# Kernel tuning notes

Measured on AMD Instinct MI355X. Metric: run time of the kernel, lower is better.

The kernel has to match this reference:

```python
import jax, jax.numpy as jnp
import numpy as np

BN_EPS = 0.001
ALPHA = 10.0
WEIGHT_BIT = 8
ACT_BIT = 8
BIAS_BIT = 16


def _ste_round(x, s):
    # straight-through quantize: round(x*s)/s with identity gradient
    return x + jax.lax.stop_gradient(jnp.round(x * s) / s - x)


def _qsym(x, bit):
    # symmetric per-tensor 'scale' quantization
    s = (2.0 ** (bit - 1) - 1.0) / jnp.maximum(jnp.max(jnp.abs(x)), 1e-8)
    return _ste_round(x, s)


def _qrelu(x, alpha, bit):
    # clipped ReLU to [0, alpha] then uniform quantization to 2^bit - 1 levels
    y = jnp.clip(x, 0.0, alpha)
    s = (2.0 ** bit - 1.0) / alpha
    return _ste_round(y, s)


def _folded_qconv(x, w, b, gamma, beta, mean, var, stride, pad):
    # fold BN into conv weights/bias, then quantize weight (8b) and bias (16b)
    sc = gamma / jnp.sqrt(var + BN_EPS)            # [O]
    wf = _qsym(w * sc[:, None, None, None], WEIGHT_BIT)
    bf = _qsym((b - mean) * sc + beta, BIAS_BIT)
    y = jax.lax.conv_general_dilated(
        x, wf, window_strides=stride, padding=[(pad, pad), (pad, pad)],
        dimension_numbers=('NCHW', 'OIHW', 'NCHW'))
    return y + bf[None, :, None, None]


def setup_inputs() -> dict:
    key = jax.random.key(0)
    ks = jax.random.split(key, 20)
    Cin, Cmid, Cout = 256, 128, 512
    d = {'x': jax.random.normal(ks[0], (32, Cin, 56, 56), dtype=jnp.float32)}

    def mk(k0, o, i, kh, kw, tag):
        kk = jax.random.split(k0, 6)
        fan = i * kh * kw
        d['w' + tag] = jax.random.normal(kk[0], (o, i, kh, kw), jnp.float32) * (fan ** -0.5)
        d['b' + tag] = jax.random.normal(kk[1], (o,), jnp.float32) * 0.01
        d['g' + tag] = 1.0 + jax.random.normal(kk[2], (o,), jnp.float32) * 0.1
        d['be' + tag] = jax.random.normal(kk[3], (o,), jnp.float32) * 0.1
        d['m' + tag] = jax.random.normal(kk[4], (o,), jnp.float32) * 0.1
        d['v' + tag] = jax.random.uniform(kk[5], (o,), jnp.float32) + 0.5

    mk(ks[1], Cmid, Cin, 1, 1, '1')
    mk(ks[2], Cmid, Cmid, 3, 3, '2')
    mk(ks[3], Cout, Cmid, 1, 1, '3')
    return d


def reference(x, w1, b1, g1, be1, m1, v1,
              w2, b2, g2, be2, m2, v2,
              w3, b3, g3, be3, m3, v3):
    out = _folded_qconv(x, w1, b1, g1, be1, m1, v1, (1, 1), 0)
    out = _qrelu(out, ALPHA, ACT_BIT)
    out = _folded_qconv(out, w2, b2, g2, be2, m2, v2, (1, 1), 1)
    out = _qrelu(out, ALPHA, ACT_BIT)
    out = _folded_qconv(out, w3, b3, g3, be3, m3, v3, (1, 1), 0)
    return out
```

## Files before the change

### kernel.cpp

```cpp
#include <hip/hip_runtime.h>
#include <math.h>

typedef int v4i  __attribute__((ext_vector_type(4)));
typedef int v16i __attribute__((ext_vector_type(16)));
typedef short v8s __attribute__((ext_vector_type(8)));
typedef float v16f __attribute__((ext_vector_type(16)));

#define N_IMG 32
#define CIN   256
#define CMID  128
#define COUT  512
#define HWP   3136
#define W58   58
#define PLANE_Q 3456
#define CBSTRIDE (PLANE_Q*16)
#define IMGSTRIDE (8*CBSTRIDE)
#define BSROW 248
#define GUARD 16384
#define BN_EPS_F 1e-3f
#define ALPHA_F  10.0f
#define ARELU_S  25.5f

#define OFF_WQ1   0
#define OFF_WF2   32768
#define OFF_WF3   180224
#define OFF_BQ1   245760
#define OFF_BQ2   245888
#define OFF_BQ3   246016
#define OFF_MAX   246528
#define OFF_Q2    246536
#define OFF_Q3    246664
#define OFF_WQ2I  247296
#define OFF_WQ3I  284160
#define OFF_WBF1  300544
#define ACT1Q_GUARD_B 52582400u
#define ACT1Q_B       (ACT1Q_GUARD_B + GUARD)
#define ACT2Q_B       (ACT1Q_B + (unsigned)(N_IMG*IMGSTRIDE) + GUARD)

__device__ __forceinline__ void async16(const char* g, char* l) {
    __builtin_amdgcn_global_load_lds((const __attribute__((address_space(1))) void*)g,
                                     (__attribute__((address_space(3))) void*)l, 16, 0, 0);
}

__global__ __launch_bounds__(256) void fold_all_kernel(
    const float* __restrict__ w1, const float* __restrict__ g1, const float* __restrict__ v1,
    const float* __restrict__ w2, const float* __restrict__ g2, const float* __restrict__ v2,
    const float* __restrict__ w3, const float* __restrict__ g3, const float* __restrict__ v3,
    const float* __restrict__ b1, const float* __restrict__ be1, const float* __restrict__ m1,
    const float* __restrict__ b2, const float* __restrict__ be2, const float* __restrict__ m2,
    const float* __restrict__ b3, const float* __restrict__ be3, const float* __restrict__ m3,
    float* __restrict__ wq1, float* __restrict__ wf2, float* __restrict__ wf3,
    float* __restrict__ bq1, float* __restrict__ bq2, float* __restrict__ bq3,
    unsigned int* __restrict__ maxw)
{
    __shared__ float red[256];
    const int b = blockIdx.x, t = threadIdx.x;
    if (b < 960) {
        const float *w, *g, *v; float* wf; int inner; unsigned int* mslot; int i;
        if (b < 128)      { w = w1; g = g1; v = v1; wf = wq1; inner = CIN;      mslot = maxw + 0; i = b * 256 + t; }
        else if (b < 704) { w = w2; g = g2; v = v2; wf = wf2; inner = CMID * 9; mslot = maxw + 1; i = (b - 128) * 256 + t; }
        else              { w = w3; g = g3; v = v3; wf = wf3; inner = CMID;     mslot = maxw + 2; i = (b - 704) * 256 + t; }
        int o = i / inner;
        float sc = g[o] / sqrtf(v[o] + BN_EPS_F);
        float val = w[i] * sc;
        wf[i] = val;
        red[t] = fabsf(val);
        __syncthreads();
        for (int s = 128; s > 0; s >>= 1) {
            if (t < s) red[t] = fmaxf(red[t], red[t + s]);
            __syncthreads();
        }
        if (t == 0) atomicMax(mslot, __float_as_uint(red[0]));
    } else {
        const float *bb, *gg, *bebe, *mm, *vv; float* bq; int nn;
        if (b == 960)      { bb = b1; gg = g1; bebe = be1; mm = m1; vv = v1; bq = bq1; nn = CMID; }
        else if (b == 961) { bb = b2; gg = g2; bebe = be2; mm = m2; vv = v2; bq = bq2; nn = CMID; }
        else               { bb = b3; gg = g3; bebe = be3; mm = m3; vv = v3; bq = bq3; nn = COUT; }
        float val0 = 0.f, val1 = 0.f;
        if (t < nn) {
            float sc = gg[t] / sqrtf(vv[t] + BN_EPS_F);
            val0 = (bb[t] - mm[t]) * sc + bebe[t];
        }
        int t2 = t + 256;
        if (t2 < nn) {
            float sc = gg[t2] / sqrtf(vv[t2] + BN_EPS_F);
            val1 = (bb[t2] - mm[t2]) * sc + bebe[t2];
        }
        red[t] = fmaxf(fabsf(val0), fabsf(val1));
        __syncthreads();
        for (int s = 128; s > 0; s >>= 1) {
            if (t < s) red[t] = fmaxf(red[t], red[t + s]);
            __syncthreads();
        }
        float mx = fmaxf(red[0], 1e-8f);
        float s = 32767.0f / mx;
        if (t < nn)  bq[t]  = rintf(val0 * s) / s;
        if (t2 < nn) bq[t2] = rintf(val1 * s) / s;
    }
}

__global__ __launch_bounds__(256) void quant_all_kernel(
    const float* __restrict__ wq1f, const float* __restrict__ wf2, const float* __restrict__ wf3,
    const unsigned int* __restrict__ maxw,
    unsigned short* __restrict__ wbf, char* __restrict__ wq2i, char* __restrict__ wq3i,
    int* __restrict__ Q2, int* __restrict__ Q3)
{
    __shared__ int red[256];
    const int b = blockIdx.x, t = threadIdx.x;
    if (b < 128) {
        int i = b * 256 + t;
        float s = 127.0f / fmaxf(__uint_as_float(maxw[0]), 1e-8f);
        int kb = i >> 10, rem = i & 1023;
        int m = rem >> 3, j = rem & 7;
        int c = kb * 8 + j;
        float k = rintf(wq1f[m * CIN + c] * s);
        wbf[i] = (unsigned short)(__float_as_uint(k) >> 16);
    } else if (b < 256) {
        int m = b - 128;
        float s = 127.0f / fmaxf(__uint_as_float(maxw[1]), 1e-8f);
        int sum = 0;
        for (int idx = t; idx < CMID * 9; idx += 256) {
            int c = idx / 9, tap = idx - c * 9;
            int q = (int)rintf(wf2[(size_t)m * (CMID * 9) + idx] * s);
            wq2i[(size_t)tap * 16384 + (c >> 4) * 2048 + m * 16 + (c & 15)] = (char)q;
            sum += q;
        }
        red[t] = sum;
        __syncthreads();
        for (int st = 128; st > 0; st >>= 1) {
            if (t < st) red[t] += red[t + st];
            __syncthreads();
        }
        if (t == 0) Q2[m] = red[0];
    } else {
        int m = (b - 256) * 2 + (t >> 7), c = t & 127;
        float s = 127.0f / fmaxf(__uint_as_float(maxw[2]), 1e-8f);
        int q = (int)rintf(wf3[(size_t)m * CMID + c] * s);
        wq3i[(size_t)(c >> 4) * 8192 + m * 16 + (c & 15)] = (char)q;
        red[t] = q;
        __syncthreads();
        for (int st = 64; st > 0; st >>= 1) {
            if ((t & 127) < st) red[t] += red[t + st];
            __syncthreads();
        }
        if ((t & 127) == 0) Q3[m] = red[t];
    }
}

__global__ __launch_bounds__(256) void conv1_bf16_kernel(
    const float* __restrict__ X, const unsigned short* __restrict__ Wbf,
    const unsigned int* __restrict__ maxw, const float* __restrict__ bq1,
    char* __restrict__ act1q)
{
    __shared__ char lds[49152];
    char* Bh = lds;
    char* Bm = lds + 16384;
    char* Bl = lds + 32768;
    const int tid = threadIdx.x;
    const int n  = blockIdx.z;
    const int q0 = blockIdx.x * 128;
    const int lane = tid & 63, wid = tid >> 6;
    const int lo = lane & 31, hi = lane >> 5;
    const int wm = wid >> 1, wn = wid & 1;
    const float* Xn = X + (size_t)n * CIN * HWP;

    const int skb = tid >> 5, sqq = tid & 31;
    const int qq0 = q0 + sqq * 4;
    int p_[4];
#pragma unroll
    for (int e = 0; e < 4; e++) {
        int q = qq0 + e;
        int y = q / W58, xx = q - y * W58;
        int p = (y - 1) * 56 + (xx - 1);
        p_[e] = p < 0 ? 0 : (p > HWP - 1 ? HWP - 1 : p);
    }
    const bool fast = (p_[1] == p_[0] + 1) && (p_[2] == p_[0] + 2) && (p_[3] == p_[0] + 3);

    v16f acc[2][2] = {};

    for (int kc = 0; kc < 4; kc++) {
        __syncthreads();
        const float* chbase = Xn + (size_t)(kc * 64 + skb * 8) * HWP;
        float v[8][4];
#pragma unroll
        for (int j = 0; j < 8; j++) {
            const float* cp = chbase + (size_t)j * HWP;
            if (fast) {
                float4 f = *(const float4*)(cp + p_[0]);
                v[j][0] = f.x; v[j][1] = f.y; v[j][2] = f.z; v[j][3] = f.w;
            } else {
#pragma unroll
                for (int e = 0; e < 4; e++) v[j][e] = cp[p_[e]];
            }
        }
#pragma unroll
        for (int e = 0; e < 4; e++) {
            unsigned ph[4], pm_[4], pl[4];
#pragma unroll
            for (int jj = 0; jj < 4; jj++) {
                float a0 = v[2 * jj][e], a1 = v[2 * jj + 1][e];
                unsigned u0 = __float_as_uint(a0), u1 = __float_as_uint(a1);
                unsigned h0 = u0 & 0xFFFF0000u, h1 = u1 & 0xFFFF0000u;
                float r0 = a0 - __uint_as_float(h0), r1 = a1 - __uint_as_float(h1);
                unsigned w0 = __float_as_uint(r0) & 0xFFFF0000u;
                unsigned w1 = __float_as_uint(r1) & 0xFFFF0000u;
                float s0 = r0 - __uint_as_float(w0), s1 = r1 - __uint_as_float(w1);
                unsigned l0 = __float_as_uint(s0) & 0xFFFF0000u;
                unsigned l1 = __float_as_uint(s1) & 0xFFFF0000u;
                ph[jj]  = (h0 >> 16) | h1;
                pm_[jj] = (w0 >> 16) | w1;
                pl[jj]  = (l0 >> 16) | l1;
            }
            int off = (skb * 128 + sqq * 4 + e) * 16;
            *(uint4*)(Bh + off) = make_uint4(ph[0], ph[1], ph[2], ph[3]);
            *(uint4*)(Bm + off) = make_uint4(pm_[0], pm_[1], pm_[2], pm_[3]);
            *(uint4*)(Bl + off) = make_uint4(pl[0], pl[1], pl[2], pl[3]);
        }
        __syncthreads();

        const char* wbase = (const char*)Wbf + kc * 16384;
#pragma unroll
        for (int ks = 0; ks < 4; ks++) {
            v8s a[2];
#pragma unroll
            for (int s = 0; s < 2; s++)
                a[s] = *(const v8s*)(wbase + (((ks * 2 + hi) * 128) + wm * 64 + s * 32 + lo) * 16);
#pragma unroll
            for (int pass = 0; pass < 3; pass++) {
                const char* Bp = (pass == 0) ? Bh : ((pass == 1) ? Bm : Bl);
                v8s b[2];
#pragma unroll
                for (int t = 0; t < 2; t++)
                    b[t] = *(const v8s*)(Bp + ((ks * 2 + hi) * 128 + wn * 64 + t * 32 + lo) * 16);
#pragma unroll
                for (int s = 0; s < 2; s++)
#pragma unroll
                    for (int t = 0; t < 2; t++)
                        acc[s][t] = __builtin_amdgcn_mfma_f32_32x32x16_bf16(a[s], b[t], acc[s][t], 0, 0, 0);
            }
        }
    }

    float inv_s = fmaxf(__uint_as_float(maxw[0]), 1e-8f) / 127.0f;
    __syncthreads();
    char* Cs = lds;
#pragma unroll
    for (int s = 0; s < 2; s++)
#pragma unroll
        for (int t = 0; t < 2; t++) {
            int qloc = wn * 64 + t * 32 + lo;
#pragma unroll
            for (int reg = 0; reg < 16; reg++) {
                int m = wm * 64 + s * 32 + (reg & 3) + 8 * (reg >> 2) + 4 * hi;
                float val = fmaf(acc[s][t][reg], inv_s, bq1[m]);
                val = fminf(fmaxf(val, 0.f), ALPHA_F);
                int k1 = (int)rintf(val * ARELU_S);
                Cs[qloc * 148 + m] = (char)(k1 - 128);
            }
        }
    __syncthreads();
    char* dst = act1q + (size_t)n * IMGSTRIDE + (size_t)q0 * 16;
#pragma unroll
    for (int it = 0; it < 4; it++) {
        int idx = it * 256 + tid;
        int ql = idx >> 3, cb = idx & 7;
        int q = q0 + ql;
        int y = q / W58, xx = q - y * W58;
        int4 w;
        if ((unsigned)(y - 1) < 56u && (unsigned)(xx - 1) < 56u) {
            w.x = *(const int*)(Cs + ql * 148 + cb * 16 + 0);
            w.y = *(const int*)(Cs + ql * 148 + cb * 16 + 4);
            w.z = *(const int*)(Cs + ql * 148 + cb * 16 + 8);
            w.w = *(const int*)(Cs + ql * 148 + cb * 16 + 12);
        } else {
            w = make_int4(0x80808080, 0x80808080, 0x80808080, 0x80808080);
        }
        *(int4*)(dst + (size_t)cb * CBSTRIDE + ql * 16) = w;
    }
}

__global__ __launch_bounds__(256) void conv2_i8_kernel(
    const char* __restrict__ actq, const char* __restrict__ wq2i,
    const int* __restrict__ Q2, const float* __restrict__ bq2,
    const unsigned int* __restrict__ maxw, char* __restrict__ act2q)
{
    __shared__ char lds[31744];
    char* Bs = lds;
    const int tid = threadIdx.x;
    const int n  = blockIdx.z;
    const int q0 = blockIdx.x * 128;
    const int lane = tid & 63, wid = tid >> 6;
    const int lo = lane & 31, hi = lane >> 5;
    const int wm = wid >> 1, wn = wid & 1;

    const char* src = actq + (size_t)n * IMGSTRIDE + (long)(q0 - 59) * 16;
#pragma unroll
    for (int cb = 0; cb < 8; cb++) {
        if (tid < 246)
            async16(src + (size_t)cb * CBSTRIDE + tid * 16, Bs + cb * (BSROW * 16) + tid * 16);
    }
    __syncthreads();

    v16i acc[2][2] = {};
    for (int tap = 0; tap < 9; tap++) {
        const char* wt = wq2i + (size_t)tap * 16384;
        const int tapoff = ((tap / 3) - 1) * W58 + (tap % 3) - 1;
#pragma unroll
        for (int ks = 0; ks < 4; ks++) {
            v4i a[2], b[2];
#pragma unroll
            for (int s = 0; s < 2; s++)
                a[s] = *(const v4i*)(wt + (ks * 2 + hi) * 2048 + (wm * 64 + s * 32 + lo) * 16);
#pragma unroll
            for (int t = 0; t < 2; t++) {
                int ql = 59 + tapoff + wn * 64 + t * 32 + lo;
                b[t] = *(const v4i*)(Bs + ((ks * 2 + hi) * BSROW + ql) * 16);
            }
#pragma unroll
            for (int s = 0; s < 2; s++)
#pragma unroll
                for (int t = 0; t < 2; t++)
                    acc[s][t] = __builtin_amdgcn_mfma_i32_32x32x32_i8(a[s], b[t], acc[s][t], 0, 0, 0);
        }
    }

    float scale = fmaxf(__uint_as_float(maxw[1]), 1e-8f) / (127.0f * ARELU_S);
    __syncthreads();
    char* Cs = lds;
#pragma unroll
    for (int s = 0; s < 2; s++)
#pragma unroll
        for (int t = 0; t < 2; t++) {
            int qloc = wn * 64 + t * 32 + lo;
#pragma unroll
            for (int reg = 0; reg < 16; reg++) {
                int m = wm * 64 + s * 32 + (reg & 3) + 8 * (reg >> 2) + 4 * hi;
                float val = fmaf((float)(acc[s][t][reg] + 128 * Q2[m]), scale, bq2[m]);
                val = fminf(fmaxf(val, 0.f), ALPHA_F);
                int k2 = (int)rintf(val * ARELU_S);
                Cs[qloc * 148 + m] = (char)(k2 - 128);
            }
        }
    __syncthreads();
    char* dst = act2q + (size_t)n * IMGSTRIDE + q0 * 16;
#pragma unroll
    for (int it = 0; it < 4; it++) {
        int idx = it * 256 + tid;
        int q = idx >> 3, cb = idx & 7;
        int4 w;
        w.x = *(const int*)(Cs + q * 148 + cb * 16 + 0);
        w.y = *(const int*)(Cs + q * 148 + cb * 16 + 4);
        w.z = *(const int*)(Cs + q * 148 + cb * 16 + 8);
        w.w = *(const int*)(Cs + q * 148 + cb * 16 + 12);
        *(int4*)(dst + (size_t)cb * CBSTRIDE + q * 16) = w;
    }
}

__global__ __launch_bounds__(256) void conv3_i8_kernel(
    const char* __restrict__ act2q, const char* __restrict__ wq3i,
    const int* __restrict__ Q3, const float* __restrict__ bq3,
    const unsigned int* __restrict__ maxw, float* __restrict__ out)
{
    __shared__ char lds[16384];
    char* Bs = lds;
    const int tid = threadIdx.x;
    const int n  = blockIdx.z;
    const int q0 = blockIdx.x * 128;
    const int m0 = blockIdx.y * 128;
    const int lane = tid & 63, wid = tid >> 6;
    const int lo = lane & 31, hi = lane >> 5;
    const int wm = wid >> 1, wn = wid & 1;

    const char* bsrc = act2q + (size_t)n * IMGSTRIDE + q0 * 16;
#pragma unroll
    for (int i = 0; i < 4; i++) {
        int cb = i * 2 + (tid >> 7), row = tid & 127;
        async16(bsrc + (size_t)cb * CBSTRIDE + row * 16, Bs + cb * 2048 + row * 16);
    }
    __syncthreads();

    v16i acc[2][2] = {};
#pragma unroll
    for (int ks = 0; ks < 4; ks++) {
        v4i a[2], b[2];
#pragma unroll
        for (int s = 0; s < 2; s++)
            a[s] = *(const v4i*)(wq3i + (ks * 2 + hi) * 8192 + (m0 + wm * 64 + s * 32 + lo) * 16);
#pragma unroll
        for (int t = 0; t < 2; t++)
            b[t] = *(const v4i*)(Bs + ((ks * 2 + hi) * 128 + wn * 64 + t * 32 + lo) * 16);
#pragma unroll
        for (int s = 0; s < 2; s++)
#pragma unroll
            for (int t = 0; t < 2; t++)
                acc[s][t] = __builtin_amdgcn_mfma_i32_32x32x32_i8(a[s], b[t], acc[s][t], 0, 0, 0);
    }

    float scale = fmaxf(__uint_as_float(maxw[2]), 1e-8f) / (127.0f * ARELU_S);
#pragma unroll
    for (int s = 0; s < 2; s++)
#pragma unroll
        for (int t = 0; t < 2; t++) {
            int q = q0 + wn * 64 + t * 32 + lo;
            int y = q / W58, x = q - y * W58;
            if ((unsigned)(y - 1) < 56u && (unsigned)(x - 1) < 56u) {
                int p = (y - 1) * 56 + (x - 1);
                float* op = out + (size_t)n * COUT * HWP + p;
#pragma unroll
                for (int reg = 0; reg < 16; reg++) {
                    int m = m0 + wm * 64 + s * 32 + (reg & 3) + 8 * (reg >> 2) + 4 * hi;
                    op[(size_t)m * HWP] = fmaf((float)(acc[s][t][reg] + 128 * Q3[m]), scale, bq3[m]);
                }
            }
        }
}

extern "C" void kernel_launch(void* const* d_in, const int* in_sizes, int n_in,
                              void* d_out, int out_size, void* d_ws, size_t ws_size,
                              hipStream_t stream) {
    const float* x   = (const float*)d_in[0];
    const float* w1  = (const float*)d_in[1];
    const float* b1  = (const float*)d_in[2];
    const float* g1  = (const float*)d_in[3];
    const float* be1 = (const float*)d_in[4];
    const float* m1  = (const float*)d_in[5];
    const float* v1  = (const float*)d_in[6];
    const float* w2  = (const float*)d_in[7];
    const float* b2  = (const float*)d_in[8];
    const float* g2  = (const float*)d_in[9];
    const float* be2 = (const float*)d_in[10];
    const float* m2  = (const float*)d_in[11];
    const float* v2  = (const float*)d_in[12];
    const float* w3  = (const float*)d_in[13];
    const float* b3  = (const float*)d_in[14];
    const float* g3  = (const float*)d_in[15];
    const float* be3 = (const float*)d_in[16];
    const float* m3  = (const float*)d_in[17];
    const float* v3  = (const float*)d_in[18];

    float* ws  = (float*)d_ws;
    unsigned char* wsb = (unsigned char*)d_ws;
    float* wq1 = ws + OFF_WQ1;
    float* wf2 = ws + OFF_WF2;
    float* wf3 = ws + OFF_WF3;
    float* bq1 = ws + OFF_BQ1;
    float* bq2 = ws + OFF_BQ2;
    float* bq3 = ws + OFF_BQ3;
    unsigned int* maxw = (unsigned int*)(ws + OFF_MAX);
    int* Q2 = (int*)(ws + OFF_Q2);
    int* Q3 = (int*)(ws + OFF_Q3);
    char* wq2i = (char*)(ws + OFF_WQ2I);
    char* wq3i = (char*)(ws + OFF_WQ3I);
    unsigned short* wbf = (unsigned short*)(ws + OFF_WBF1);
    char* act1q = (char*)(wsb + ACT1Q_B);
    char* act2q = (char*)(wsb + ACT2Q_B);
    float* out  = (float*)d_out;

    hipMemsetAsync(maxw, 0, 12, stream);

    fold_all_kernel<<<963, 256, 0, stream>>>(
        w1, g1, v1, w2, g2, v2, w3, g3, v3,
        b1, be1, m1, b2, be2, m2, b3, be3, m3,
        wq1, wf2, wf3, bq1, bq2, bq3, maxw);

    quant_all_kernel<<<512, 256, 0, stream>>>(wq1, wf2, wf3, maxw, wbf, wq2i, wq3i, Q2, Q3);

    conv1_bf16_kernel<<<dim3(27, 1, 32), 256, 0, stream>>>(x, wbf, maxw, bq1, act1q);
    conv2_i8_kernel<<<dim3(27, 1, 32), 256, 0, stream>>>(act1q, wq2i, Q2, bq2, maxw, act2q);
    conv3_i8_kernel<<<dim3(27, 4, 32), 256, 0, stream>>>(act2q, wq3i, Q3, bq3, maxw, out);
}
```

Baseline: 455.1 us.

## Fuse conv2 and conv3 into one kernel keeping act2 tile in LDS

Merges the 3x3 int8 conv2 kernel with the 1x1 conv3 kernel. Each block now quantizes its conv2 output tile into LDS and immediately runs conv3 over all four 128-channel output slices, holding the B fragments in registers. This removes the global write and reread of the act2 intermediate and one kernel launch. In exchange, the grid for conv3 work drops from 3456 to 864 blocks, LDS use rises to about 47KB, and register pressure goes up, all of which may lower occupancy and parallelism for the output-store-heavy conv3 phase.

```diff
diff --git a/kernel.cpp b/kernel.cpp
--- a/kernel.cpp
+++ b/kernel.cpp
@@ -35,7 +35,6 @@
 #define OFF_WBF1  300544
 #define ACT1Q_GUARD_B 52582400u
 #define ACT1Q_B       (ACT1Q_GUARD_B + GUARD)
-#define ACT2Q_B       (ACT1Q_B + (unsigned)(N_IMG*IMGSTRIDE) + GUARD)
 
 __device__ __forceinline__ void async16(const char* g, char* l) {
     __builtin_amdgcn_global_load_lds((const __attribute__((address_space(1))) void*)g,
@@ -279,13 +278,16 @@
     }
 }
 
-__global__ __launch_bounds__(256) void conv2_i8_kernel(
+__global__ __launch_bounds__(256) void conv23_i8_kernel(
     const char* __restrict__ actq, const char* __restrict__ wq2i,
+    const char* __restrict__ wq3i,
     const int* __restrict__ Q2, const float* __restrict__ bq2,
-    const unsigned int* __restrict__ maxw, char* __restrict__ act2q)
+    const int* __restrict__ Q3, const float* __restrict__ bq3,
+    const unsigned int* __restrict__ maxw, float* __restrict__ out)
 {
-    __shared__ char lds[31744];
+    __shared__ char lds[48128];
     char* Bs = lds;
+    char* Ps = lds + 31744;
     const int tid = threadIdx.x;
     const int n  = blockIdx.z;
     const int q0 = blockIdx.x * 128;
@@ -324,7 +326,7 @@
         }
     }
 
-    float scale = fmaxf(__uint_as_float(maxw[1]), 1e-8f) / (127.0f * ARELU_S);
+    float scale2 = fmaxf(__uint_as_float(maxw[1]), 1e-8f) / (127.0f * ARELU_S);
     __syncthreads();
     char* Cs = lds;
 #pragma unroll
@@ -335,84 +337,68 @@
 #pragma unroll
             for (int reg = 0; reg < 16; reg++) {
                 int m = wm * 64 + s * 32 + (reg & 3) + 8 * (reg >> 2) + 4 * hi;
-                float val = fmaf((float)(acc[s][t][reg] + 128 * Q2[m]), scale, bq2[m]);
+                float val = fmaf((float)(acc[s][t][reg] + 128 * Q2[m]), scale2, bq2[m]);
                 val = fminf(fmaxf(val, 0.f), ALPHA_F);
                 int k2 = (int)rintf(val * ARELU_S);
                 Cs[qloc * 148 + m] = (char)(k2 - 128);
             }
         }
     __syncthreads();
-    char* dst = act2q + (size_t)n * IMGSTRIDE + q0 * 16;
 #pragma unroll
     for (int it = 0; it < 4; it++) {
         int idx = it * 256 + tid;
-        int q = idx >> 3, cb = idx & 7;
+        int cb = idx >> 7, q = idx & 127;
         int4 w;
         w.x = *(const int*)(Cs + q * 148 + cb * 16 + 0);
         w.y = *(const int*)(Cs + q * 148 + cb * 16 + 4);
         w.z = *(const int*)(Cs + q * 148 + cb * 16 + 8);
         w.w = *(const int*)(Cs + q * 148 + cb * 16 + 12);
-        *(int4*)(dst + (size_t)cb * CBSTRIDE + q * 16) = w;
-    }
-}
-
-__global__ __launch_bounds__(256) void conv3_i8_kernel(
-    const char* __restrict__ act2q, const char* __restrict__ wq3i,
-    const int* __restrict__ Q3, const float* __restrict__ bq3,
-    const unsigned int* __restrict__ maxw, float* __restrict__ out)
-{
-    __shared__ char lds[16384];
-    char* Bs = lds;
-    const int tid = threadIdx.x;
-    const int n  = blockIdx.z;
-    const int q0 = blockIdx.x * 128;
-    const int m0 = blockIdx.y * 128;
-    const int lane = tid & 63, wid = tid >> 6;
-    const int lo = lane & 31, hi = lane >> 5;
-    const int wm = wid >> 1, wn = wid & 1;
-
-    const char* bsrc = act2q + (size_t)n * IMGSTRIDE + q0 * 16;
-#pragma unroll
-    for (int i = 0; i < 4; i++) {
-        int cb = i * 2 + (tid >> 7), row = tid & 127;
-        async16(bsrc + (size_t)cb * CBSTRIDE + row * 16, Bs + cb * 2048 + row * 16);
-    }
-    __syncthreads();
-
-    v16i acc[2][2] = {};
-#pragma unroll
-    for (int ks = 0; ks < 4; ks++) {
-        v4i a[2], b[2];
+        *(int4*)(Ps + cb * 2048 + q * 16) = w;
+    }
+    __syncthreads();
+
+    float scale3 = fmaxf(__uint_as_float(maxw[2]), 1e-8f) / (127.0f * ARELU_S);
+    v4i bf[4][2];
+#pragma unroll
+    for (int ks = 0; ks < 4; ks++)
+#pragma unroll
+        for (int t = 0; t < 2; t++)
+            bf[ks][t] = *(const v4i*)(Ps + (ks * 2 + hi) * 2048 + (wn * 64 + t * 32 + lo) * 16);
+
+    const int qq = q0 + wn * 64 + lo;
+#pragma unroll
+    for (int m0i = 0; m0i < 4; m0i++) {
+        const int m0 = m0i * 128;
+        v16i acc3[2][2] = {};
+#pragma unroll
+        for (int ks = 0; ks < 4; ks++) {
+            v4i a[2];
+#pragma unroll
+            for (int s = 0; s < 2; s++)
+                a[s] = *(const v4i*)(wq3i + (ks * 2 + hi) * 8192 + (m0 + wm * 64 + s * 32 + lo) * 16);
+#pragma unroll
+            for (int s = 0; s < 2; s++)
+#pragma unroll
+                for (int t = 0; t < 2; t++)
+                    acc3[s][t] = __builtin_amdgcn_mfma_i32_32x32x32_i8(a[s], bf[ks][t], acc3[s][t], 0, 0, 0);
+        }
 #pragma unroll
         for (int s = 0; s < 2; s++)
-            a[s] = *(const v4i*)(wq3i + (ks * 2 + hi) * 8192 + (m0 + wm * 64 + s * 32 + lo) * 16);
-#pragma unroll
-        for (int t = 0; t < 2; t++)
-            b[t] = *(const v4i*)(Bs + ((ks * 2 + hi) * 128 + wn * 64 + t * 32 + lo) * 16);
-#pragma unroll
-        for (int s = 0; s < 2; s++)
-#pragma unroll
-            for (int t = 0; t < 2; t++)
-                acc[s][t] = __builtin_amdgcn_mfma_i32_32x32x32_i8(a[s], b[t], acc[s][t], 0, 0, 0);
-    }
-
-    float scale = fmaxf(__uint_as_float(maxw[2]), 1e-8f) / (127.0f * ARELU_S);
-#pragma unroll
-    for (int s = 0; s < 2; s++)
-#pragma unroll
-        for (int t = 0; t < 2; t++) {
-            int q = q0 + wn * 64 + t * 32 + lo;
-            int y = q / W58, x = q - y * W58;
-            if ((unsigned)(y - 1) < 56u && (unsigned)(x - 1) < 56u) {
-                int p = (y - 1) * 56 + (x - 1);
-                float* op = out + (size_t)n * COUT * HWP + p;
-#pragma unroll
-                for (int reg = 0; reg < 16; reg++) {
-                    int m = m0 + wm * 64 + s * 32 + (reg & 3) + 8 * (reg >> 2) + 4 * hi;
-                    op[(size_t)m * HWP] = fmaf((float)(acc[s][t][reg] + 128 * Q3[m]), scale, bq3[m]);
+#pragma unroll
+            for (int t = 0; t < 2; t++) {
+                int q = qq + t * 32;
+                int y = q / W58, x = q - y * W58;
+                if ((unsigned)(y - 1) < 56u && (unsigned)(x - 1) < 56u) {
+                    int p = (y - 1) * 56 + (x - 1);
+                    float* op = out + (size_t)n * COUT * HWP + p;
+#pragma unroll
+                    for (int reg = 0; reg < 16; reg++) {
+                        int m = m0 + wm * 64 + s * 32 + (reg & 3) + 8 * (reg >> 2) + 4 * hi;
+                        op[(size_t)m * HWP] = fmaf((float)(acc3[s][t][reg] + 128 * Q3[m]), scale3, bq3[m]);
+                    }
                 }
             }
-        }
+    }
 }
 
 extern "C" void kernel_launch(void* const* d_in, const int* in_sizes, int n_in,
@@ -453,7 +439,6 @@
     char* wq3i = (char*)(ws + OFF_WQ3I);
     unsigned short* wbf = (unsigned short*)(ws + OFF_WBF1);
     char* act1q = (char*)(wsb + ACT1Q_B);
-    char* act2q = (char*)(wsb + ACT2Q_B);
     float* out  = (float*)d_out;
 
     hipMemsetAsync(maxw, 0, 12, stream);
@@ -466,6 +451,5 @@
     quant_all_kernel<<<512, 256, 0, stream>>>(wq1, wf2, wf3, maxw, wbf, wq2i, wq3i, Q2, Q3);
 
     conv1_bf16_kernel<<<dim3(27, 1, 32), 256, 0, stream>>>(x, wbf, maxw, bq1, act1q);
-    conv2_i8_kernel<<<dim3(27, 1, 32), 256, 0, stream>>>(act1q, wq2i, Q2, bq2, maxw, act2q);
-    conv3_i8_kernel<<<dim3(27, 4, 32), 256, 0, stream>>>(act2q, wq3i, Q3, bq3, maxw, out);
-}
+    conv23_i8_kernel<<<dim3(27, 1, 32), 256, 0, stream>>>(act1q, wq2i, wq3i, Q2, bq2, Q3, bq3, maxw, out);
+}
```

New measurement: 445.0 us. -2.2%, faster.
